# Kernel tuning notes

Hardware: AMD Instinct MI355X
Metric: run time of the kernel (lower is better)

The kernel has to match this reference:

```python
import jax, jax.numpy as jnp
import numpy as np

H = 32     # hidden_size
S = 64     # sequence length (steps)


def positional_encoding(seq_len, d_model):
    # faithful to source: position * div_term with div_term = 10000**(arange/ d)
    position = jnp.arange(seq_len, dtype=jnp.float32)[:, None]
    div_term = 10000.0 ** (jnp.arange(0, d_model, 2, dtype=jnp.float32) / d_model)
    ang = position * div_term                      # [S, H/2]
    pe = jnp.zeros((seq_len, d_model), dtype=jnp.float32)
    pe = pe.at[:, 0::2].set(jnp.sin(ang))
    pe = pe.at[:, 1::2].set(jnp.cos(ang))
    return pe                                      # [seq_len, H]


def setup_inputs() -> dict:
    key = jax.random.key(0)
    ks = jax.random.split(key, 6)
    B, K, NP, V = 32, 64, 100000, 4096
    return {
        "neighbor_ids": jax.random.randint(ks[0], (B, S, K, 2), 0, V, dtype=jnp.int32),
        "param_indices": jax.random.randint(ks[1], (B, S, K), 0, NP, dtype=jnp.int32),
        "weights": jax.random.uniform(ks[2], (NP, H, H), minval=-0.5, maxval=0.5, dtype=jnp.float32),
        "biases": jax.random.uniform(ks[3], (NP, H), minval=-0.5, maxval=0.5, dtype=jnp.float32),
        "node_bias": jax.random.uniform(ks[4], (V, H), minval=-0.5, maxval=0.5, dtype=jnp.float32),
        "positions": jnp.ones((512,), dtype=jnp.float32),
    }


def reference(neighbor_ids, param_indices, weights, biases, node_bias, positions):
    B = neighbor_ids.shape[0]
    gelu = lambda x: jax.nn.gelu(x, approximate=False)  # torch nn.GELU default (erf)
    pe = positional_encoding(512, H)                    # [512, H]

    # initial energy: ones/H + node_bias[src of first edge] + pe[0]
    init_energy = gelu(1.0 / H + node_bias[neighbor_ids[:, 0, 0, 0]] + pe[0])  # [B, H]

    pos_logits = positions[:S]        # [S]
    steps = jnp.arange(S)

    def step(carry, i):
        cache, loss_sum = carry       # cache: [B, S, H] (rows >= i are zero)
        # softmax pooling over the growing cache (positions[:i])
        mask = steps < i
        w = jax.nn.softmax(jnp.where(mask, pos_logits, -1e30))  # [S]
        pooled = jnp.einsum('s,bsh->bh', w, cache)              # [B, H]
        energy = jnp.where(i == 0, init_energy, pooled)         # [B, H]

        idx = jax.lax.dynamic_index_in_dim(param_indices, i, axis=1, keepdims=False)  # [B, K]
        Wm = weights[idx]            # [B, K, H, H] per-edge weight gather
        bm = biases[idx]             # [B, K, H]
        nxt = gelu(jnp.einsum('bh,bkhd->bkd', energy, Wm) + bm + pe[i + 1])  # [B, K, H]

        enorm = jnp.linalg.norm(nxt, axis=-1)                   # [B, K]
        # CrossEntropy with label 0
        loss_i = jnp.mean(jax.nn.logsumexp(enorm, axis=1) - enorm[:, 0])
        cache = cache.at[:, i, :].set(nxt[:, 0])                # append gold-edge output
        return (cache, loss_sum + loss_i), None

    cache0 = jnp.zeros((B, S, H), dtype=jnp.float32)
    (_, loss_sum), _ = jax.lax.scan(step, (cache0, jnp.float32(0.0)), steps)
    return loss_sum / S
```

## Files before the change

### kernel.cpp

```cpp
#include <hip/hip_runtime.h>
#include <math.h>

#define H 32
#define S 64
#define K 64
#define B 32

__device__ __forceinline__ float gelu_f(float x) {
    return 0.5f * x * (1.0f + erff(x * 0.70710678118654752440f));
}

__device__ __forceinline__ void lds_fence() {
    asm volatile("s_waitcnt lgkmcnt(0)" ::: "memory");
}

__device__ __forceinline__ float bcast_lane(float v, int lane) {
    return __uint_as_float(__builtin_amdgcn_readlane(__float_as_uint(v), lane));
}


__global__ void precompute_kernel(float* __restrict__ pe) {
    int t = blockIdx.x * 256 + threadIdx.x;
    if (t < 65 * 32) {
        int p = t >> 5, c = t & 31;
        int iq = c >> 1;
        double dt = pow(10000.0, (double)(2 * iq) / 32.0);
        float ang = (float)p * (float)dt;
        double v = (c & 1) ? cos((double)ang) : sin((double)ang);
        pe[t] = (float)v;
    }
}

__global__ __launch_bounds__(64) void chain_kernel(
    const int* __restrict__ neighbor_ids,
    const int* __restrict__ param_indices,
    const float* __restrict__ weights,
    const float* __restrict__ biases,
    const float* __restrict__ node_bias,
    const float* __restrict__ pe_g,
    const float* __restrict__ positions,
    float* __restrict__ energies) {
    int b = blockIdx.x;
    int l = threadIdx.x;
    int r = l >> 5;
    int d = l & 31;

    __shared__ int idx_sh[S];
    __shared__ float pos_sh[S];
    __shared__ float pe_sh[(S + 1) * H];
    __shared__ float bias_sh[S * H];

    idx_sh[l] = param_indices[((size_t)(b * S + l)) * K];
    pos_sh[l] = positions[l];
    for (int t = l; t < (S + 1) * H; t += 64) pe_sh[t] = pe_g[t];
    lds_fence();

    for (int t = l; t < S * H; t += 64)
        bias_sh[t] = biases[(size_t)idx_sh[t >> 5] * H + (t & 31)];

    float init_e;
    {
        int nid = neighbor_ids[(size_t)b * S * K * 2];
        init_e = gelu_f(0.03125f + node_bias[(size_t)nid * H + d] + pe_sh[d]);
    }
    lds_fence();

    float w0[16], w1[16], w2[16], w3[16];
    const int rowoff = r * 16;

    auto loadW = [&](float (&wb)[16], int step) {
        const float* Wp = weights + (size_t)idx_sh[step] * (H * H) + (size_t)rowoff * H + d;
        #pragma unroll
        for (int j = 0; j < 16; ++j) wb[j] = Wp[j * H];
    };
    loadW(w0, 0); loadW(w1, 1); loadW(w2, 2); loadW(w3, 3);

    float m = -1e30f, ssum = 0.0f, A = 0.0f, nxtprev = 0.0f;

    auto step = [&](float (&wb)[16], int i) {
        float e;
        if (i == 0) {
            e = init_e;
        } else {
            float p = pos_sh[i - 1];
            if (p > m) { float sc = expf(m - p); A *= sc; ssum *= sc; m = p; }
            float wgt = expf(p - m);
            A = fmaf(wgt, nxtprev, A);
            ssum += wgt;
            e = A / ssum;
        }
        if (r == 0) energies[((size_t)(b * S + i)) * H + d] = e;

        float acc = 0.0f;
        #pragma unroll
        for (int j = 0; j < 16; ++j) {
            float e0 = bcast_lane(e, j);
            float e1 = bcast_lane(e, 16 + j);
            acc = fmaf(r ? e1 : e0, wb[j], acc);
        }
        acc += __shfl_xor(acc, 32, 64);
        nxtprev = gelu_f(acc + bias_sh[i * H + d] + pe_sh[(i + 1) * H + d]);
        if (i + 4 < S) loadW(wb, i + 4);
    };

    #pragma unroll
    for (int ii = 0; ii < S; ii += 4) {
        step(w0, ii);
        step(w1, ii + 1);
        step(w2, ii + 2);
        step(w3, ii + 3);
    }
}

__global__ __launch_bounds__(256) void big_kernel(
    const int* __restrict__ param_indices,
    const float* __restrict__ weights,
    const float* __restrict__ biases,
    const float* __restrict__ pe_g,
    const float* __restrict__ energies,
    float* __restrict__ partials) {
    int bi = blockIdx.x;
    int i = bi & 63;
    int tid = threadIdx.x;
    int wave = tid >> 6;
    int lane = tid & 63;
    int q = lane >> 4;
    int dp = lane & 15;

    __shared__ float e_sh[H];
    __shared__ float en_sh[K];
    __shared__ int idx_sh[K];

    if (tid < H) e_sh[tid] = energies[(size_t)bi * H + tid];
    if (tid < K) idx_sh[tid] = param_indices[(size_t)bi * K + tid];
    float pex = pe_g[(i + 1) * H + 2 * dp];
    float pey = pe_g[(i + 1) * H + 2 * dp + 1];
    __syncthreads();

    float ereg[8];
    #pragma unroll
    for (int hh = 0; hh < 8; ++hh) ereg[hh] = e_sh[hh * 4 + q];

    int ka0 = wave * 16;

    float2 ca[8], cb[8], bca, bcb;
    {
        int ia = idx_sh[ka0], ib = idx_sh[ka0 + 8];
        const float2* Wa = (const float2*)(weights + (size_t)ia * (H * H));
        const float2* Wb = (const float2*)(weights + (size_t)ib * (H * H));
        #pragma unroll
        for (int hh = 0; hh < 8; ++hh) {
            ca[hh] = Wa[(hh * 4 + q) * 16 + dp];
            cb[hh] = Wb[(hh * 4 + q) * 16 + dp];
        }
        bca = *(const float2*)(biases + (size_t)ia * H + 2 * dp);
        bcb = *(const float2*)(biases + (size_t)ib * H + 2 * dp);
    }

    #pragma unroll
    for (int it = 0; it < 8; ++it) {
        float2 na[8], nb[8], bna, bnb;
        if (it < 7) {
            int ia = idx_sh[ka0 + it + 1], ib = idx_sh[ka0 + 8 + it + 1];
            const float2* Wa = (const float2*)(weights + (size_t)ia * (H * H));
            const float2* Wb = (const float2*)(weights + (size_t)ib * (H * H));
            #pragma unroll
            for (int hh = 0; hh < 8; ++hh) {
                na[hh] = Wa[(hh * 4 + q) * 16 + dp];
                nb[hh] = Wb[(hh * 4 + q) * 16 + dp];
            }
            bna = *(const float2*)(biases + (size_t)ia * H + 2 * dp);
            bnb = *(const float2*)(biases + (size_t)ib * H + 2 * dp);
        }

        float axa = 0, aya = 0, axb = 0, ayb = 0;
        #pragma unroll
        for (int hh = 0; hh < 8; ++hh) {
            axa = fmaf(ereg[hh], ca[hh].x, axa);
            aya = fmaf(ereg[hh], ca[hh].y, aya);
            axb = fmaf(ereg[hh], cb[hh].x, axb);
            ayb = fmaf(ereg[hh], cb[hh].y, ayb);
        }
        axa += __shfl_xor(axa, 16, 64); aya += __shfl_xor(aya, 16, 64);
        axb += __shfl_xor(axb, 16, 64); ayb += __shfl_xor(ayb, 16, 64);
        axa += __shfl_xor(axa, 32, 64); aya += __shfl_xor(aya, 32, 64);
        axb += __shfl_xor(axb, 32, 64); ayb += __shfl_xor(ayb, 32, 64);
        float v0a = gelu_f(axa + bca.x + pex);
        float v1a = gelu_f(aya + bca.y + pey);
        float v0b = gelu_f(axb + bcb.x + pex);
        float v1b = gelu_f(ayb + bcb.y + pey);
        float ssa = fmaf(v0a, v0a, v1a * v1a);
        float ssb = fmaf(v0b, v0b, v1b * v1b);
        #pragma unroll
        for (int mk = 8; mk; mk >>= 1) {
            ssa += __shfl_xor(ssa, mk, 64);
            ssb += __shfl_xor(ssb, mk, 64);
        }
        if (lane == 0) { en_sh[ka0 + it] = sqrtf(ssa); en_sh[ka0 + 8 + it] = sqrtf(ssb); }

        if (it < 7) {
            #pragma unroll
            for (int hh = 0; hh < 8; ++hh) { ca[hh] = na[hh]; cb[hh] = nb[hh]; }
            bca = bna; bcb = bnb;
        }
    }
    __syncthreads();

    if (tid < K) {
        float en = en_sh[tid];
        float mm = en;
        #pragma unroll
        for (int mk = 32; mk; mk >>= 1) mm = fmaxf(mm, __shfl_xor(mm, mk, 64));
        float s = expf(en - mm);
        #pragma unroll
        for (int mk = 32; mk; mk >>= 1) s += __shfl_xor(s, mk, 64);
        if (tid == 0) partials[bi] = mm + logf(s) - en_sh[0];
    }
}

__global__ __launch_bounds__(256) void reduce_kernel(const float* __restrict__ partials,
                                                     float* __restrict__ out) {
    __shared__ float sh[256];
    int tid = threadIdx.x;
    float s = 0.0f;
    for (int j = 0; j < 8; ++j) s += partials[tid + j * 256];
    sh[tid] = s;
    __syncthreads();
    for (int ofs = 128; ofs; ofs >>= 1) {
        if (tid < ofs) sh[tid] += sh[tid + ofs];
        __syncthreads();
    }
    if (tid == 0) out[0] = sh[0] * (1.0f / 2048.0f);
}

extern "C" void kernel_launch(void* const* d_in, const int* in_sizes, int n_in,
                              void* d_out, int out_size, void* d_ws, size_t ws_size,
                              hipStream_t stream) {
    const int*   neighbor_ids  = (const int*)d_in[0];
    const int*   param_indices = (const int*)d_in[1];
    const float* weights       = (const float*)d_in[2];
    const float* biases        = (const float*)d_in[3];
    const float* node_bias     = (const float*)d_in[4];
    const float* positions     = (const float*)d_in[5];

    float* ws       = (float*)d_ws;
    float* pe       = ws;
    float* energies = ws + 2080;
    float* partials = ws + 2080 + B * S * H;

    hipLaunchKernelGGL(precompute_kernel, dim3(9), dim3(256), 0, stream, pe);
    hipLaunchKernelGGL(chain_kernel, dim3(B), dim3(64), 0, stream,
                       neighbor_ids, param_indices, weights, biases, node_bias,
                       pe, positions, energies);
    hipLaunchKernelGGL(big_kernel, dim3(B * S), dim3(256), 0, stream,
                       param_indices, weights, biases, pe, energies, partials);
    hipLaunchKernelGGL(reduce_kernel, dim3(1), dim3(256), 0, stream,
                       partials, (float*)d_out);
}
```

Baseline: 135.1 us.

## Fuse chain, edge-scoring and reduce into one persistent kernel with flag-based overlap

After: 222.4 us. +64.6%, slower.

```diff
diff --git a/kernel.cpp b/kernel.cpp
--- a/kernel.cpp
+++ b/kernel.cpp
@@ -5,6 +5,9 @@
 #define S 64
 #define K 64
 #define B 32
+#define NTILE 2048
+#define GRID 512
+#define NBIGW (GRID * 4 - 32)
 
 __device__ __forceinline__ float gelu_f(float x) {
     return 0.5f * x * (1.0f + erff(x * 0.70710678118654752440f));
@@ -19,8 +22,11 @@
 }
 
 
-__global__ void precompute_kernel(float* __restrict__ pe) {
+__global__ void precompute_kernel(float* __restrict__ pe, int* __restrict__ flags,
+                                  int* __restrict__ ctr) {
     int t = blockIdx.x * 256 + threadIdx.x;
+    if (t == 0) ctr[0] = 0;
+    if (t < NTILE) flags[t] = 0;
     if (t < 65 * 32) {
         int p = t >> 5, c = t & 31;
         int iq = c >> 1;
@@ -31,7 +37,7 @@
     }
 }
 
-__global__ __launch_bounds__(64) void chain_kernel(
+__global__ __launch_bounds__(256, 2) void fused_kernel(
     const int* __restrict__ neighbor_ids,
     const int* __restrict__ param_indices,
     const float* __restrict__ weights,
@@ -39,198 +45,221 @@
     const float* __restrict__ node_bias,
     const float* __restrict__ pe_g,
     const float* __restrict__ positions,
-    float* __restrict__ energies) {
-    int b = blockIdx.x;
-    int l = threadIdx.x;
-    int r = l >> 5;
-    int d = l & 31;
-
-    __shared__ int idx_sh[S];
-    __shared__ float pos_sh[S];
-    __shared__ float pe_sh[(S + 1) * H];
-    __shared__ float bias_sh[S * H];
-
-    idx_sh[l] = param_indices[((size_t)(b * S + l)) * K];
-    pos_sh[l] = positions[l];
-    for (int t = l; t < (S + 1) * H; t += 64) pe_sh[t] = pe_g[t];
-    lds_fence();
-
-    for (int t = l; t < S * H; t += 64)
-        bias_sh[t] = biases[(size_t)idx_sh[t >> 5] * H + (t & 31)];
-
-    float init_e;
-    {
-        int nid = neighbor_ids[(size_t)b * S * K * 2];
-        init_e = gelu_f(0.03125f + node_bias[(size_t)nid * H + d] + pe_sh[d]);
+    float* __restrict__ energies,
+    float* __restrict__ partials,
+    int* __restrict__ flags,
+    int* __restrict__ ctr,
+    float* __restrict__ out) {
+    const int bid = blockIdx.x;
+    const int tid = threadIdx.x;
+    const int wv = tid >> 6;
+    const int lane = tid & 63;
+    const int gw = bid * 4 + wv;
+
+    __shared__ int c_idx[S];
+    __shared__ float c_pos[S];
+    __shared__ float c_pe[(S + 1) * H];
+    __shared__ float c_bias[S * H];
+    __shared__ float en_sh[4][K];
+    __shared__ float red_sh[256];
+
+    if (bid < 32 && wv == 0) {
+        const int b = bid;
+        const int l = lane;
+        const int r = l >> 5;
+        const int d = l & 31;
+
+        c_idx[l] = param_indices[((size_t)(b * S + l)) * K];
+        c_pos[l] = positions[l];
+        for (int t = l; t < (S + 1) * H; t += 64) c_pe[t] = pe_g[t];
+        lds_fence();
+
+        for (int t = l; t < S * H; t += 64)
+            c_bias[t] = biases[(size_t)c_idx[t >> 5] * H + (t & 31)];
+
+        float w0[16], w1[16], w2[16], w3[16];
+        const int rowoff = r * 16;
+        auto loadW = [&](float (&wb)[16], int step) {
+            const float* Wp = weights + (size_t)c_idx[step] * (H * H) + (size_t)rowoff * H + d;
+            #pragma unroll
+            for (int j = 0; j < 16; ++j) wb[j] = Wp[j * H];
+        };
+        loadW(w0, 0); loadW(w1, 1); loadW(w2, 2); loadW(w3, 3);
+
+        float init_e;
+        {
+            int nid = neighbor_ids[(size_t)b * S * K * 2];
+            init_e = gelu_f(0.03125f + node_bias[(size_t)nid * H + d] + c_pe[d]);
+        }
+        lds_fence();
+
+        float m = -1e30f, ssum = 0.0f, A = 0.0f, nxtprev = 0.0f;
+
+        auto step = [&](float (&wb)[16], int i) {
+            float e;
+            if (i == 0) {
+                e = init_e;
+            } else {
+                float p = c_pos[i - 1];
+                if (p > m) { float sc = expf(m - p); A *= sc; ssum *= sc; m = p; }
+                float wgt = expf(p - m);
+                A = fmaf(wgt, nxtprev, A);
+                ssum += wgt;
+                e = A / ssum;
+            }
+            if (r == 0)
+                __hip_atomic_store(&energies[((size_t)(b * S + i)) * H + d], e,
+                                   __ATOMIC_RELAXED, __HIP_MEMORY_SCOPE_AGENT);
+            if (l == 0)
+                __hip_atomic_store(&flags[i * 32 + b], 1,
+                                   __ATOMIC_RELEASE, __HIP_MEMORY_SCOPE_AGENT);
+            if (i + 4 < S) loadW(wb, i + 4);
+
+            float a0 = 0.0f, a1 = 0.0f, a2 = 0.0f, a3 = 0.0f;
+            #pragma unroll
+            for (int j = 0; j < 4; ++j) {
+                float e0, e1;
+                e0 = bcast_lane(e, 4 * j + 0); e1 = bcast_lane(e, 16 + 4 * j + 0);
+                a0 = fmaf(r ? e1 : e0, wb[4 * j + 0], a0);
+                e0 = bcast_lane(e, 4 * j + 1); e1 = bcast_lane(e, 16 + 4 * j + 1);
+                a1 = fmaf(r ? e1 : e0, wb[4 * j + 1], a1);
+                e0 = bcast_lane(e, 4 * j + 2); e1 = bcast_lane(e, 16 + 4 * j + 2);
+                a2 = fmaf(r ? e1 : e0, wb[4 * j + 2], a2);
+                e0 = bcast_lane(e, 4 * j + 3); e1 = bcast_lane(e, 16 + 4 * j + 3);
+                a3 = fmaf(r ? e1 : e0, wb[4 * j + 3], a3);
+            }
+            float acc = (a0 + a1) + (a2 + a3);
+            acc += __shfl_xor(acc, 32, 64);
+            nxtprev = gelu_f(acc + c_bias[i * H + d] + c_pe[(i + 1) * H + d]);
+        };
+
+        #pragma unroll
+        for (int ii = 0; ii < S; ii += 4) {
+            step(w0, ii); step(w1, ii + 1); step(w2, ii + 2); step(w3, ii + 3);
+        }
+    } else {
+        int bigrank = gw - min((gw + 3) >> 2, 32);
+        const int q = lane >> 4;
+        const int dp = lane & 15;
+
+        for (int t = bigrank; t < NTILE; t += NBIGW) {
+            const int b = t & 31, i = t >> 5;
+            const int bi = b * S + i;
+
+            if (__hip_atomic_load(&flags[t], __ATOMIC_RELAXED, __HIP_MEMORY_SCOPE_AGENT) == 0) {
+                do { __builtin_amdgcn_s_sleep(2); }
+                while (__hip_atomic_load(&flags[t], __ATOMIC_RELAXED, __HIP_MEMORY_SCOPE_AGENT) == 0);
+            }
+
+            float pex = pe_g[(i + 1) * H + 2 * dp];
+            float pey = pe_g[(i + 1) * H + 2 * dp + 1];
+            int idxv = param_indices[(size_t)bi * K + lane];
+            float ereg[8];
+            #pragma unroll
+            for (int hh = 0; hh < 8; ++hh)
+                ereg[hh] = __hip_atomic_load(&energies[(size_t)bi * H + hh * 4 + q],
+                                             __ATOMIC_RELAXED, __HIP_MEMORY_SCOPE_AGENT);
+
+            int ia = __builtin_amdgcn_readlane(idxv, 0);
+            int ib = __builtin_amdgcn_readlane(idxv, 32);
+            float2 ca[8], cb[8], bca, bcb;
+            {
+                const float2* Wa = (const float2*)(weights + (size_t)ia * (H * H));
+                const float2* Wb = (const float2*)(weights + (size_t)ib * (H * H));
+                #pragma unroll
+                for (int hh = 0; hh < 8; ++hh) {
+                    ca[hh] = Wa[(hh * 4 + q) * 16 + dp];
+                    cb[hh] = Wb[(hh * 4 + q) * 16 + dp];
+                }
+                bca = *(const float2*)(biases + (size_t)ia * H + 2 * dp);
+                bcb = *(const float2*)(biases + (size_t)ib * H + 2 * dp);
+            }
+
+            for (int it = 0; it < 32; ++it) {
+                float2 na[8], nb[8], bna, bnb;
+                if (it < 31) {
+                    int ja = __builtin_amdgcn_readlane(idxv, it + 1);
+                    int jb = __builtin_amdgcn_readlane(idxv, it + 33);
+                    const float2* Wa = (const float2*)(weights + (size_t)ja * (H * H));
+                    const float2* Wb = (const float2*)(weights + (size_t)jb * (H * H));
+                    #pragma unroll
+                    for (int hh = 0; hh < 8; ++hh) {
+                        na[hh] = Wa[(hh * 4 + q) * 16 + dp];
+                        nb[hh] = Wb[(hh * 4 + q) * 16 + dp];
+                    }
+                    bna = *(const float2*)(biases + (size_t)ja * H + 2 * dp);
+                    bnb = *(const float2*)(biases + (size_t)jb * H + 2 * dp);
+                }
+
+                float axa = 0, aya = 0, axb = 0, ayb = 0;
+                #pragma unroll
+                for (int hh = 0; hh < 8; ++hh) {
+                    axa = fmaf(ereg[hh], ca[hh].x, axa);
+                    aya = fmaf(ereg[hh], ca[hh].y, aya);
+                    axb = fmaf(ereg[hh], cb[hh].x, axb);
+                    ayb = fmaf(ereg[hh], cb[hh].y, ayb);
+                }
+                axa += __shfl_xor(axa, 16, 64); aya += __shfl_xor(aya, 16, 64);
+                axb += __shfl_xor(axb, 16, 64); ayb += __shfl_xor(ayb, 16, 64);
+                axa += __shfl_xor(axa, 32, 64); aya += __shfl_xor(aya, 32, 64);
+                axb += __shfl_xor(axb, 32, 64); ayb += __shfl_xor(ayb, 32, 64);
+                float v0a = gelu_f(axa + bca.x + pex);
+                float v1a = gelu_f(aya + bca.y + pey);
+                float v0b = gelu_f(axb + bcb.x + pex);
+                float v1b = gelu_f(ayb + bcb.y + pey);
+                float ssa = fmaf(v0a, v0a, v1a * v1a);
+                float ssb = fmaf(v0b, v0b, v1b * v1b);
+                #pragma unroll
+                for (int mk = 8; mk; mk >>= 1) {
+                    ssa += __shfl_xor(ssa, mk, 64);
+                    ssb += __shfl_xor(ssb, mk, 64);
+                }
+                if (lane == 0) {
+                    en_sh[wv][it]      = sqrtf(ssa);
+                    en_sh[wv][it + 32] = sqrtf(ssb);
+                }
+                if (it < 31) {
+                    #pragma unroll
+                    for (int hh = 0; hh < 8; ++hh) { ca[hh] = na[hh]; cb[hh] = nb[hh]; }
+                    bca = bna; bcb = bnb;
+                }
+            }
+            lds_fence();
+            float en = en_sh[wv][lane];
+            float mm = en;
+            #pragma unroll
+            for (int mk = 32; mk; mk >>= 1) mm = fmaxf(mm, __shfl_xor(mm, mk, 64));
+            float sx = expf(en - mm);
+            #pragma unroll
+            for (int mk = 32; mk; mk >>= 1) sx += __shfl_xor(sx, mk, 64);
+            float en0 = bcast_lane(en, 0);
+            if (lane == 0)
+                __hip_atomic_store(&partials[bi], mm + logf(sx) - en0,
+                                   __ATOMIC_RELAXED, __HIP_MEMORY_SCOPE_AGENT);
+        }
     }
-    lds_fence();
-
-    float w0[16], w1[16], w2[16], w3[16];
-    const int rowoff = r * 16;
-
-    auto loadW = [&](float (&wb)[16], int step) {
-        const float* Wp = weights + (size_t)idx_sh[step] * (H * H) + (size_t)rowoff * H + d;
-        #pragma unroll
-        for (int j = 0; j < 16; ++j) wb[j] = Wp[j * H];
-    };
-    loadW(w0, 0); loadW(w1, 1); loadW(w2, 2); loadW(w3, 3);
-
-    float m = -1e30f, ssum = 0.0f, A = 0.0f, nxtprev = 0.0f;
-
-    auto step = [&](float (&wb)[16], int i) {
-        float e;
-        if (i == 0) {
-            e = init_e;
-        } else {
-            float p = pos_sh[i - 1];
-            if (p > m) { float sc = expf(m - p); A *= sc; ssum *= sc; m = p; }
-            float wgt = expf(p - m);
-            A = fmaf(wgt, nxtprev, A);
-            ssum += wgt;
-            e = A / ssum;
-        }
-        if (r == 0) energies[((size_t)(b * S + i)) * H + d] = e;
-
-        float acc = 0.0f;
-        #pragma unroll
-        for (int j = 0; j < 16; ++j) {
-            float e0 = bcast_lane(e, j);
-            float e1 = bcast_lane(e, 16 + j);
-            acc = fmaf(r ? e1 : e0, wb[j], acc);
-        }
-        acc += __shfl_xor(acc, 32, 64);
-        nxtprev = gelu_f(acc + bias_sh[i * H + d] + pe_sh[(i + 1) * H + d]);
-        if (i + 4 < S) loadW(wb, i + 4);
-    };
-
-    #pragma unroll
-    for (int ii = 0; ii < S; ii += 4) {
-        step(w0, ii);
-        step(w1, ii + 1);
-        step(w2, ii + 2);
-        step(w3, ii + 3);
+
+    __syncthreads();
+    if (tid == 0)
+        __hip_atomic_fetch_add(ctr, 1, __ATOMIC_RELEASE, __HIP_MEMORY_SCOPE_AGENT);
+    if (bid == 0) {
+        if (tid == 0) {
+            while (__hip_atomic_load(ctr, __ATOMIC_RELAXED, __HIP_MEMORY_SCOPE_AGENT) < GRID)
+                __builtin_amdgcn_s_sleep(8);
+        }
+        __syncthreads();
+        float s = 0.0f;
+        for (int j = 0; j < 8; ++j)
+            s += __hip_atomic_load(&partials[tid + j * 256],
+                                   __ATOMIC_RELAXED, __HIP_MEMORY_SCOPE_AGENT);
+        red_sh[tid] = s;
+        __syncthreads();
+        for (int ofs = 128; ofs; ofs >>= 1) {
+            if (tid < ofs) red_sh[tid] += red_sh[tid + ofs];
+            __syncthreads();
+        }
+        if (tid == 0) out[0] = red_sh[0] * (1.0f / 2048.0f);
     }
-}
-
-__global__ __launch_bounds__(256) void big_kernel(
-    const int* __restrict__ param_indices,
-    const float* __restrict__ weights,
-    const float* __restrict__ biases,
-    const float* __restrict__ pe_g,
-    const float* __restrict__ energies,
-    float* __restrict__ partials) {
-    int bi = blockIdx.x;
-    int i = bi & 63;
-    int tid = threadIdx.x;
-    int wave = tid >> 6;
-    int lane = tid & 63;
-    int q = lane >> 4;
-    int dp = lane & 15;
-
-    __shared__ float e_sh[H];
-    __shared__ float en_sh[K];
-    __shared__ int idx_sh[K];
-
-    if (tid < H) e_sh[tid] = energies[(size_t)bi * H + tid];
-    if (tid < K) idx_sh[tid] = param_indices[(size_t)bi * K + tid];
-    float pex = pe_g[(i + 1) * H + 2 * dp];
-    float pey = pe_g[(i + 1) * H + 2 * dp + 1];
-    __syncthreads();
-
-    float ereg[8];
-    #pragma unroll
-    for (int hh = 0; hh < 8; ++hh) ereg[hh] = e_sh[hh * 4 + q];
-
-    int ka0 = wave * 16;
-
-    float2 ca[8], cb[8], bca, bcb;
-    {
-        int ia = idx_sh[ka0], ib = idx_sh[ka0 + 8];
-        const float2* Wa = (const float2*)(weights + (size_t)ia * (H * H));
-        const float2* Wb = (const float2*)(weights + (size_t)ib * (H * H));
-        #pragma unroll
-        for (int hh = 0; hh < 8; ++hh) {
-            ca[hh] = Wa[(hh * 4 + q) * 16 + dp];
-            cb[hh] = Wb[(hh * 4 + q) * 16 + dp];
-        }
-        bca = *(const float2*)(biases + (size_t)ia * H + 2 * dp);
-        bcb = *(const float2*)(biases + (size_t)ib * H + 2 * dp);
-    }
-
-    #pragma unroll
-    for (int it = 0; it < 8; ++it) {
-        float2 na[8], nb[8], bna, bnb;
-        if (it < 7) {
-            int ia = idx_sh[ka0 + it + 1], ib = idx_sh[ka0 + 8 + it + 1];
-            const float2* Wa = (const float2*)(weights + (size_t)ia * (H * H));
-            const float2* Wb = (const float2*)(weights + (size_t)ib * (H * H));
-            #pragma unroll
-            for (int hh = 0; hh < 8; ++hh) {
-                na[hh] = Wa[(hh * 4 + q) * 16 + dp];
-                nb[hh] = Wb[(hh * 4 + q) * 16 + dp];
-            }
-            bna = *(const float2*)(biases + (size_t)ia * H + 2 * dp);
-            bnb = *(const float2*)(biases + (size_t)ib * H + 2 * dp);
-        }
-
-        float axa = 0, aya = 0, axb = 0, ayb = 0;
-        #pragma unroll
-        for (int hh = 0; hh < 8; ++hh) {
-            axa = fmaf(ereg[hh], ca[hh].x, axa);
-            aya = fmaf(ereg[hh], ca[hh].y, aya);
-            axb = fmaf(ereg[hh], cb[hh].x, axb);
-            ayb = fmaf(ereg[hh], cb[hh].y, ayb);
-        }
-        axa += __shfl_xor(axa, 16, 64); aya += __shfl_xor(aya, 16, 64);
-        axb += __shfl_xor(axb, 16, 64); ayb += __shfl_xor(ayb, 16, 64);
-        axa += __shfl_xor(axa, 32, 64); aya += __shfl_xor(aya, 32, 64);
-        axb += __shfl_xor(axb, 32, 64); ayb += __shfl_xor(ayb, 32, 64);
-        float v0a = gelu_f(axa + bca.x + pex);
-        float v1a = gelu_f(aya + bca.y + pey);
-        float v0b = gelu_f(axb + bcb.x + pex);
-        float v1b = gelu_f(ayb + bcb.y + pey);
-        float ssa = fmaf(v0a, v0a, v1a * v1a);
-        float ssb = fmaf(v0b, v0b, v1b * v1b);
-        #pragma unroll
-        for (int mk = 8; mk; mk >>= 1) {
-            ssa += __shfl_xor(ssa, mk, 64);
-            ssb += __shfl_xor(ssb, mk, 64);
-        }
-        if (lane == 0) { en_sh[ka0 + it] = sqrtf(ssa); en_sh[ka0 + 8 + it] = sqrtf(ssb); }
-
-        if (it < 7) {
-            #pragma unroll
-            for (int hh = 0; hh < 8; ++hh) { ca[hh] = na[hh]; cb[hh] = nb[hh]; }
-            bca = bna; bcb = bnb;
-        }
-    }
-    __syncthreads();
-
-    if (tid < K) {
-        float en = en_sh[tid];
-        float mm = en;
-        #pragma unroll
-        for (int mk = 32; mk; mk >>= 1) mm = fmaxf(mm, __shfl_xor(mm, mk, 64));
-        float s = expf(en - mm);
-        #pragma unroll
-        for (int mk = 32; mk; mk >>= 1) s += __shfl_xor(s, mk, 64);
-        if (tid == 0) partials[bi] = mm + logf(s) - en_sh[0];
-    }
-}
-
-__global__ __launch_bounds__(256) void reduce_kernel(const float* __restrict__ partials,
-                                                     float* __restrict__ out) {
-    __shared__ float sh[256];
-    int tid = threadIdx.x;
-    float s = 0.0f;
-    for (int j = 0; j < 8; ++j) s += partials[tid + j * 256];
-    sh[tid] = s;
-    __syncthreads();
-    for (int ofs = 128; ofs; ofs >>= 1) {
-        if (tid < ofs) sh[tid] += sh[tid + ofs];
-        __syncthreads();
-    }
-    if (tid == 0) out[0] = sh[0] * (1.0f / 2048.0f);
 }
 
 extern "C" void kernel_launch(void* const* d_in, const int* in_sizes, int n_in,
@@ -247,13 +276,13 @@
     float* pe       = ws;
     float* energies = ws + 2080;
     float* partials = ws + 2080 + B * S * H;
-
-    hipLaunchKernelGGL(precompute_kernel, dim3(9), dim3(256), 0, stream, pe);
-    hipLaunchKernelGGL(chain_kernel, dim3(B), dim3(64), 0, stream,
+    int*   flags    = (int*)(ws + 69664);
+    int*   ctr      = (int*)(ws + 71712);
+
+    hipLaunchKernelGGL(precompute_kernel, dim3(9), dim3(256), 0, stream,
+                       pe, flags, ctr);
+    hipLaunchKernelGGL(fused_kernel, dim3(GRID), dim3(256), 0, stream,
                        neighbor_ids, param_indices, weights, biases, node_bias,
-                       pe, positions, energies);
-    hipLaunchKernelGGL(big_kernel, dim3(B * S), dim3(256), 0, stream,
-                       param_indices, weights, biases, pe, energies, partials);
-    hipLaunchKernelGGL(reduce_kernel, dim3(1), dim3(256), 0, stream,
-                       partials, (float*)d_out);
-}
+                       pe, positions, energies, partials, flags, ctr,
+                       (float*)d_out);
+}
```

## Stage per-edge weight matrices into LDS via async global_load_lds double buffering

Applied to the files above, without the earlier changes.

After: 140.1 us. 3.6% more time.

```diff
diff --git a/kernel.cpp b/kernel.cpp
--- a/kernel.cpp
+++ b/kernel.cpp
@@ -122,17 +122,28 @@
     int bi = blockIdx.x;
     int i = bi & 63;
     int tid = threadIdx.x;
-    int wave = tid >> 6;
+    int wv = tid >> 6;
     int lane = tid & 63;
     int q = lane >> 4;
     int dp = lane & 15;
 
+    __shared__ float wslab[4][2][1024];
+    __shared__ float bias_sh[K * H];
     __shared__ float e_sh[H];
     __shared__ float en_sh[K];
     __shared__ int idx_sh[K];
 
     if (tid < H) e_sh[tid] = energies[(size_t)bi * H + tid];
     if (tid < K) idx_sh[tid] = param_indices[(size_t)bi * K + tid];
+    __syncthreads();
+
+    {
+        int k = tid >> 2, part = tid & 3;
+        const float4* bp = (const float4*)(biases + (size_t)idx_sh[k] * H + part * 8);
+        float4 b0 = bp[0], b1 = bp[1];
+        ((float4*)&bias_sh[k * H + part * 8])[0] = b0;
+        ((float4*)&bias_sh[k * H + part * 8])[1] = b1;
+    }
     float pex = pe_g[(i + 1) * H + 2 * dp];
     float pey = pe_g[(i + 1) * H + 2 * dp + 1];
     __syncthreads();
@@ -141,68 +152,53 @@
     #pragma unroll
     for (int hh = 0; hh < 8; ++hh) ereg[hh] = e_sh[hh * 4 + q];
 
-    int ka0 = wave * 16;
-
-    float2 ca[8], cb[8], bca, bcb;
-    {
-        int ia = idx_sh[ka0], ib = idx_sh[ka0 + 8];
-        const float2* Wa = (const float2*)(weights + (size_t)ia * (H * H));
-        const float2* Wb = (const float2*)(weights + (size_t)ib * (H * H));
+    const int lsw = lane ^ (((lane >> 3) & 3) << 1);
+
+    auto stage = [&](int m, int slot) {
+        int idx = idx_sh[wv * 16 + m];
+        const char* src = (const char*)(weights + (size_t)idx * (H * H)) + lsw * 16;
+        char* dst = (char*)&wslab[wv][slot][0];
+        #pragma unroll
+        for (int j = 0; j < 4; ++j) {
+            __builtin_amdgcn_global_load_lds(
+                (const __attribute__((address_space(1))) void*)(src + j * 1024),
+                (__attribute__((address_space(3))) void*)(dst + j * 1024),
+                16, 0, 0);
+        }
+    };
+
+    stage(0, 0);
+
+    #pragma unroll
+    for (int m = 0; m < 16; ++m) {
+        const int slot = m & 1;
+        if (m + 1 < 16) {
+            stage(m + 1, (m + 1) & 1);
+            asm volatile("s_waitcnt vmcnt(4)" ::: "memory");
+        } else {
+            asm volatile("s_waitcnt vmcnt(0)" ::: "memory");
+        }
+        __builtin_amdgcn_sched_barrier(0);
+
+        const char* Wl = (const char*)&wslab[wv][slot][0];
+        float ax = 0.0f, ay = 0.0f;
         #pragma unroll
         for (int hh = 0; hh < 8; ++hh) {
-            ca[hh] = Wa[(hh * 4 + q) * 16 + dp];
-            cb[hh] = Wb[(hh * 4 + q) * 16 + dp];
-        }
-        bca = *(const float2*)(biases + (size_t)ia * H + 2 * dp);
-        bcb = *(const float2*)(biases + (size_t)ib * H + 2 * dp);
-    }
-
-    #pragma unroll
-    for (int it = 0; it < 8; ++it) {
-        float2 na[8], nb[8], bna, bnb;
-        if (it < 7) {
-            int ia = idx_sh[ka0 + it + 1], ib = idx_sh[ka0 + 8 + it + 1];
-            const float2* Wa = (const float2*)(weights + (size_t)ia * (H * H));
-            const float2* Wb = (const float2*)(weights + (size_t)ib * (H * H));
-            #pragma unroll
-            for (int hh = 0; hh < 8; ++hh) {
-                na[hh] = Wa[(hh * 4 + q) * 16 + dp];
-                nb[hh] = Wb[(hh * 4 + q) * 16 + dp];
-            }
-            bna = *(const float2*)(biases + (size_t)ia * H + 2 * dp);
-            bnb = *(const float2*)(biases + (size_t)ib * H + 2 * dp);
-        }
-
-        float axa = 0, aya = 0, axb = 0, ayb = 0;
-        #pragma unroll
-        for (int hh = 0; hh < 8; ++hh) {
-            axa = fmaf(ereg[hh], ca[hh].x, axa);
-            aya = fmaf(ereg[hh], ca[hh].y, aya);
-            axb = fmaf(ereg[hh], cb[hh].x, axb);
-            ayb = fmaf(ereg[hh], cb[hh].y, ayb);
-        }
-        axa += __shfl_xor(axa, 16, 64); aya += __shfl_xor(aya, 16, 64);
-        axb += __shfl_xor(axb, 16, 64); ayb += __shfl_xor(ayb, 16, 64);
-        axa += __shfl_xor(axa, 32, 64); aya += __shfl_xor(aya, 32, 64);
-        axb += __shfl_xor(axb, 32, 64); ayb += __shfl_xor(ayb, 32, 64);
-        float v0a = gelu_f(axa + bca.x + pex);
-        float v1a = gelu_f(aya + bca.y + pey);
-        float v0b = gelu_f(axb + bcb.x + pex);
-        float v1b = gelu_f(ayb + bcb.y + pey);
-        float ssa = fmaf(v0a, v0a, v1a * v1a);
-        float ssb = fmaf(v0b, v0b, v1b * v1b);
-        #pragma unroll
-        for (int mk = 8; mk; mk >>= 1) {
-            ssa += __shfl_xor(ssa, mk, 64);
-            ssb += __shfl_xor(ssb, mk, 64);
-        }
-        if (lane == 0) { en_sh[ka0 + it] = sqrtf(ssa); en_sh[ka0 + 8 + it] = sqrtf(ssb); }
-
-        if (it < 7) {
-            #pragma unroll
-            for (int hh = 0; hh < 8; ++hh) { ca[hh] = na[hh]; cb[hh] = nb[hh]; }
-            bca = bna; bcb = bnb;
-        }
+            float2 w = *(const float2*)(Wl + hh * 512 + q * 128 + ((dp * 8) ^ (q << 5)));
+            ax = fmaf(ereg[hh], w.x, ax);
+            ay = fmaf(ereg[hh], w.y, ay);
+        }
+        ax += __shfl_xor(ax, 16, 64); ay += __shfl_xor(ay, 16, 64);
+        ax += __shfl_xor(ax, 32, 64); ay += __shfl_xor(ay, 32, 64);
+
+        const int k = wv * 16 + m;
+        float2 bv = *(const float2*)&bias_sh[k * H + 2 * dp];
+        float v0 = gelu_f(ax + bv.x + pex);
+        float v1 = gelu_f(ay + bv.y + pey);
+        float ss = fmaf(v0, v0, v1 * v1);
+        #pragma unroll
+        for (int mk = 8; mk; mk >>= 1) ss += __shfl_xor(ss, mk, 64);
+        if (lane == 0) en_sh[k] = sqrtf(ss);
     }
     __syncthreads();
 
```
